# Kernel optimization log

Hardware: AMD Instinct MI355X
Metric: run time of the kernel (lower is better)

Reference implementation:

```python
import jax, jax.numpy as jnp
import numpy as np

B, T, D, HD = 8, 2048, 1024, 64

def setup_inputs() -> dict:
    key = jax.random.key(0)
    k1, k2, k3, k4 = jax.random.split(key, 4)
    x = jax.random.normal(k1, (B, T, D), dtype=jnp.float32)
    Wq = jax.random.normal(k2, (D, HD), dtype=jnp.float32) * (D ** -0.5)
    Wk = jax.random.normal(k3, (D, HD), dtype=jnp.float32) * (D ** -0.5)
    Wv = jax.random.normal(k4, (D, HD), dtype=jnp.float32) * (D ** -0.5)
    return {"x": x, "Wq": Wq, "Wk": Wk, "Wv": Wv}

def reference(x, Wq, Wk, Wv):
    # x: [B,T,D]; projections: [D,HD]
    q = jnp.einsum('btd,dh->bth', x, Wq)
    k = jnp.einsum('btd,dh->bth', x, Wk)
    v = jnp.einsum('btd,dh->bth', x, Wv)
    hd = q.shape[-1]
    scores = jnp.einsum('bth,bsh->bts', q, k) * (hd ** -0.5)  # [B,T,T]
    t = scores.shape[-1]
    causal = jnp.tril(jnp.ones((t, t), dtype=bool))
    scores = jnp.where(causal, scores, -jnp.inf)
    w = jax.nn.softmax(scores, axis=-1)
    # dropout p=0.0 (eval) -> identity
    return jnp.einsum('bts,bsh->bth', w, v)
```

## Files before the change

kernel.cpp:

```cpp
#include <hip/hip_runtime.h>
#include <hip/hip_bf16.h>
#include <stdint.h>

#define NB 8
#define TT 2048
#define DD 1024
#define HDIM 64

typedef __bf16 bf16x8 __attribute__((ext_vector_type(8)));
typedef float f32x4 __attribute__((ext_vector_type(4)));
typedef ushort u16x4 __attribute__((ext_vector_type(4)));

static_assert(sizeof(bf16x8) == 16, "bf16x8 must be 16 bytes");

__device__ inline ushort f2bf_bits(float f) {
    __hip_bfloat16 h = __float2bfloat16(f);
    return *reinterpret_cast<ushort*>(&h);
}
__device__ inline float bfbits2f(ushort u) {
    unsigned v = ((unsigned)u) << 16;
    return __builtin_bit_cast(float, v);
}
__device__ inline bf16x8 ldb8(const ushort* p) {
    return *reinterpret_cast<const bf16x8*>(p);
}

typedef __attribute__((address_space(3))) uint32_t lds_u32;
typedef const __attribute__((address_space(1))) uint32_t glb_u32;
__device__ inline void gl_lds16(const void* g, void* l) {
    __builtin_amdgcn_global_load_lds((glb_u32*)g, (lds_u32*)l, 16, 0, 0);
}

#define WCNT_VM2   0xF72
#define WCNT_VM3   0xF73
#define WCNT_VM5   0xF75
#define WCNT_LGKM0 0xC07F

__device__ inline int probe_f32(const ushort* x) {
    int lane = threadIdx.x & 63;
    int wild = 0;
    #pragma unroll
    for (int j = 0; j < 4; ++j) {
        ushort u = x[(lane * 4 + j) * 32];
        int e = (u >> 7) & 0xFF;
        wild += (e >= 0xC0);
    }
    unsigned long long m = __ballot(wild > 0);
    return __popcll(m) > 8;
}

__global__ __launch_bounds__(256) void k_wt(const ushort* __restrict__ x,
                                            const void* __restrict__ Wq,
                                            const void* __restrict__ Wk,
                                            const void* __restrict__ Wv,
                                            ushort* __restrict__ Wt) {
    int f32m = probe_f32(x);
    int idx = blockIdx.x * 256 + threadIdx.x;
    int mat = idx >> 16;
    int rem = idx & 65535;
    int d = rem >> 6;
    int h = rem & 63;
    const void* W = (mat == 0) ? Wq : (mat == 1) ? Wk : Wv;
    float v;
    if (f32m) v = ((const float*)W)[rem];
    else      v = bfbits2f(((const ushort*)W)[rem]);
    if (mat == 0) v *= 0.18033688011112042f;
    int n    = mat * 64 + h;
    int nt   = n >> 4, ncol = n & 15;
    int kk   = d >> 6, ks = (d >> 5) & 1, qd = (d >> 3) & 3, e = d & 7;
    int f    = nt * 2 + ks;
    Wt[((size_t)(kk * 24 + f)) * 512 + (qd * 16 + ncol) * 8 + e] = f2bf_bits(v);
}

template <int F32M>
__device__ inline void proj_body(const void* __restrict__ xv,
                                 const ushort* __restrict__ Wt,
                                 ushort* __restrict__ Qw,
                                 ushort* __restrict__ Kw,
                                 ushort* __restrict__ Vtw,
                                 ushort* Bf, ushort* Afb) {
    int tid  = threadIdx.x;
    int w    = tid >> 6;
    int lane = tid & 63;
    int quad = lane >> 4;
    int col  = lane & 15;
    int mt   = w >> 2;
    int nh   = w & 3;
    int m0   = blockIdx.x * 64;

    const float*  xf = (const float*)xv;
    const ushort* xb = (const ushort*)xv;

    auto stageB = [&](int buf, int kkk) {
        int kk24 = (kkk >> 6) * 24;
        if (w < 8) {
            #pragma unroll
            for (int j = 0; j < 2; ++j) {
                int f = w * 2 + j;
                gl_lds16(Wt + ((size_t)(kk24 + f)) * 512 + lane * 8,
                         Bf + ((size_t)buf * 24 + f) * 512);
            }
        } else {
            int f = 16 + (w - 8);
            gl_lds16(Wt + ((size_t)(kk24 + f)) * 512 + lane * 8,
                     Bf + ((size_t)buf * 24 + f) * 512);
        }
    };

    int arow = m0 + w * 4 + quad;
    int aa   = (w >> 2) * 2 + (col >> 3);
    int aoff = (((col & 7) >> 1) * 16 + (w & 3) * 4 + quad) * 8
             + (col & 1) * 4;

    f32x4 ar_f;
    u16x4 ar_b;
    auto loadA = [&](int kkk) {
        if (F32M) ar_f = *reinterpret_cast<const f32x4*>(xf + (size_t)arow * DD + kkk + col * 4);
        else      ar_b = *reinterpret_cast<const u16x4*>(xb + (size_t)arow * DD + kkk + col * 4);
    };
    auto writeA = [&](int q) {
        u16x4 v;
        if (F32M) {
            #pragma unroll
            for (int j = 0; j < 4; ++j) v[j] = f2bf_bits(ar_f[j]);
        } else {
            v = ar_b;
        }
        *reinterpret_cast<u16x4*>(Afb + ((size_t)q * 8 + aa) * 512 + aoff) = v;
    };

    f32x4 acc[3];
    #pragma unroll
    for (int i = 0; i < 3; ++i) acc[i] = (f32x4){0.f,0.f,0.f,0.f};

    loadA(0);
    stageB(0, 0);
    stageB(1, 64);
    writeA(0);
    __builtin_amdgcn_s_waitcnt(WCNT_LGKM0);

    for (int t = 0; t < 16; ++t) {
        int p   = t % 3;
        int p2  = (t + 2) % 3;
        int kn1 = (t + 1 < 16) ? (t + 1) * 64 : 960;
        int kn2 = (t + 2 < 16) ? (t + 2) * 64 : 960;
        loadA(kn1);
        stageB(p2, kn2);
        if (w < 8) __builtin_amdgcn_s_waitcnt(WCNT_VM5);
        else       __builtin_amdgcn_s_waitcnt(WCNT_VM3);
        __builtin_amdgcn_s_barrier();

        int q = t & 1;
        #pragma unroll
        for (int ks = 0; ks < 2; ++ks) {
            bf16x8 a = ldb8(Afb + ((size_t)q * 8 + mt * 2 + ks) * 512 + lane * 8);
            #pragma unroll
            for (int j = 0; j < 3; ++j) {
                int nt = nh * 3 + j;
                bf16x8 b = ldb8(Bf + ((size_t)p * 24 + nt * 2 + ks) * 512 + lane * 8);
                acc[j] = __builtin_amdgcn_mfma_f32_16x16x32_bf16(a, b, acc[j], 0, 0, 0);
            }
        }
        writeA(q ^ 1);
        __builtin_amdgcn_s_waitcnt(WCNT_LGKM0);
        __builtin_amdgcn_s_barrier();
    }

    #pragma unroll
    for (int j = 0; j < 3; ++j) {
        int nt  = nh * 3 + j;
        int mat = nt >> 2;
        int h   = (nt & 3) * 16 + col;
        if (mat == 2) {
            #pragma unroll
            for (int r = 0; r < 4; ++r) {
                int row = m0 + mt * 16 + quad * 4 + r;
                int bb = row >> 11;
                int t  = row & (TT - 1);
                Vtw[(size_t)bb * HDIM * TT + (size_t)h * TT + t] = f2bf_bits(acc[j][r]);
            }
        } else {
            ushort* outp = (mat == 0) ? Qw : Kw;
            #pragma unroll
            for (int r = 0; r < 4; ++r) {
                int row = m0 + mt * 16 + quad * 4 + r;
                outp[(size_t)row * HDIM + h] = f2bf_bits(acc[j][r]);
            }
        }
    }
}

__global__ __launch_bounds__(1024) void k_proj(const void* __restrict__ xv,
                                               const ushort* __restrict__ Wt,
                                               ushort* __restrict__ Qw,
                                               ushort* __restrict__ Kw,
                                               ushort* __restrict__ Vtw) {
    __shared__ ushort Bf[3 * 24 * 512];
    __shared__ ushort Afb[2 * 8 * 512];
    if (probe_f32((const ushort*)xv)) proj_body<1>(xv, Wt, Qw, Kw, Vtw, Bf, Afb);
    else                              proj_body<0>(xv, Wt, Qw, Kw, Vtw, Bf, Afb);
}

__global__ __launch_bounds__(256) void k_attn(const ushort* __restrict__ Qw,
                                              const ushort* __restrict__ Kw,
                                              const ushort* __restrict__ Vtw,
                                              ushort* __restrict__ Po,
                                              float* __restrict__ Pl) {
    int w    = threadIdx.x >> 6;
    int lane = threadIdx.x & 63;
    int quad = lane >> 4;
    int col  = lane & 15;
    int bid  = blockIdx.x;
    int b    = bid & 7;
    int idx  = 79 - (bid >> 3);
    int c, g;
    if (idx < 32)      { c = 0; g = idx; }
    else if (idx < 56) { c = 1; g = idx - 24; }
    else if (idx < 72) { c = 2; g = idx - 40; }
    else               { c = 3; g = idx - 48; }
    int qb = 4 * g + w;
    int m0 = qb * 16;
    int Bq = (qb < 32) ? qb : (qb < 64) ? 2*qb - 32 : (qb < 96) ? 3*qb - 96 : 4*qb - 192;
    int pid = b * 320 + Bq + c;

    const ushort* Qb = Qw + (size_t)b * TT * HDIM;
    const ushort* Kb = Kw + (size_t)b * TT * HDIM;
    const ushort* Vb = Vtw + (size_t)b * HDIM * TT;

    __shared__ ushort KVb[2][8][512];
    __shared__ __hip_bfloat16 Pls[4][16][40];

    auto stageKV = [&](int buf, int s) {
        #pragma unroll
        for (int j = 0; j < 2; ++j) {
            int f = w * 2 + j;
            const ushort* gp;
            if (f < 4) {
                int half = f & 1;
                int ro   = (f >> 1) * 16;
                gp = Kb + (size_t)(s + ro + col) * HDIM + half * 32 + quad * 8;
            } else {
                int vg = f - 4;
                gp = Vb + (size_t)(vg * 16 + col) * TT + s + quad * 8;
            }
            gl_lds16(gp, &KVb[buf][f][0]);
        }
    };

    bf16x8 qf0 = ldb8(Qb + (size_t)(m0 + col) * HDIM + quad * 8);
    bf16x8 qf1 = ldb8(Qb + (size_t)(m0 + col) * HDIM + 32 + quad * 8);

    f32x4 o0 = {0.f,0.f,0.f,0.f};
    f32x4 o1 = {0.f,0.f,0.f,0.f};
    f32x4 o2 = {0.f,0.f,0.f,0.f};
    f32x4 o3 = {0.f,0.f,0.f,0.f};
    float rsum[4] = {0.f, 0.f, 0.f, 0.f};

    const int start = c * 512;
    const int end   = min(start + 512, 64 * g + 64);

    stageKV(0, start);
    for (int s0 = start; s0 < end; s0 += 32) {
        int p  = ((s0 - start) >> 5) & 1;
        int sn = (s0 + 32 < end) ? s0 + 32 : s0;
        stageKV(p ^ 1, sn);
        __builtin_amdgcn_s_waitcnt(WCNT_VM2);
        __builtin_amdgcn_s_barrier();

        if (s0 < m0 + 16) {
            bf16x8 ck0l = ldb8(&KVb[p][0][lane * 8]);
            bf16x8 ck0h = ldb8(&KVb[p][1][lane * 8]);
            bf16x8 ck1l = ldb8(&KVb[p][2][lane * 8]);
            bf16x8 ck1h = ldb8(&KVb[p][3][lane * 8]);

            f32x4 S0 = {0.f,0.f,0.f,0.f};
            f32x4 S1 = {0.f,0.f,0.f,0.f};
            S0 = __builtin_amdgcn_mfma_f32_16x16x32_bf16(qf0, ck0l, S0, 0, 0, 0);
            S0 = __builtin_amdgcn_mfma_f32_16x16x32_bf16(qf1, ck0h, S0, 0, 0, 0);
            S1 = __builtin_amdgcn_mfma_f32_16x16x32_bf16(qf0, ck1l, S1, 0, 0, 0);
            S1 = __builtin_amdgcn_mfma_f32_16x16x32_bf16(qf1, ck1h, S1, 0, 0, 0);

            #pragma unroll
            for (int r = 0; r < 4; ++r) {
                int trow = m0 + quad * 4 + r;
                float aa = (s0 + col      > trow) ? -1e30f : S0[r];
                float dd = (s0 + 16 + col > trow) ? -1e30f : S1[r];
                float p0 = exp2f(aa);
                float p1 = exp2f(dd);
                rsum[r] += p0 + p1;
                Pls[w][quad * 4 + r][col]      = __float2bfloat16(p0);
                Pls[w][quad * 4 + r][16 + col] = __float2bfloat16(p1);
            }
            bf16x8 pf = *reinterpret_cast<const bf16x8*>(&Pls[w][col][quad * 8]);

            bf16x8 cv0 = ldb8(&KVb[p][4][lane * 8]);
            bf16x8 cv1 = ldb8(&KVb[p][5][lane * 8]);
            bf16x8 cv2 = ldb8(&KVb[p][6][lane * 8]);
            bf16x8 cv3 = ldb8(&KVb[p][7][lane * 8]);
            o0 = __builtin_amdgcn_mfma_f32_16x16x32_bf16(pf, cv0, o0, 0, 0, 0);
            o1 = __builtin_amdgcn_mfma_f32_16x16x32_bf16(pf, cv1, o1, 0, 0, 0);
            o2 = __builtin_amdgcn_mfma_f32_16x16x32_bf16(pf, cv2, o2, 0, 0, 0);
            o3 = __builtin_amdgcn_mfma_f32_16x16x32_bf16(pf, cv3, o3, 0, 0, 0);
        }
        __builtin_amdgcn_s_waitcnt(WCNT_LGKM0);
        __builtin_amdgcn_s_barrier();
    }

    #pragma unroll
    for (int off = 1; off < 16; off <<= 1) {
        #pragma unroll
        for (int r = 0; r < 4; ++r)
            rsum[r] += __shfl_xor(rsum[r], off, 64);
    }

    ushort* pb = Po + (size_t)pid * 1024;
    #pragma unroll
    for (int r = 0; r < 4; ++r) {
        int row = quad * 4 + r;
        pb[row * 64 + 0*16 + col] = f2bf_bits(o0[r]);
        pb[row * 64 + 1*16 + col] = f2bf_bits(o1[r]);
        pb[row * 64 + 2*16 + col] = f2bf_bits(o2[r]);
        pb[row * 64 + 3*16 + col] = f2bf_bits(o3[r]);
        if (col == 0) Pl[pid * 16 + row] = rsum[r];
    }
}

__global__ __launch_bounds__(256) void k_merge(const ushort* __restrict__ x,
                                               const ushort* __restrict__ Po,
                                               const float* __restrict__ Pl,
                                               void* __restrict__ outv) {
    int f32m = probe_f32(x);
    int wid  = blockIdx.x * 4 + (threadIdx.x >> 6);
    int lane = threadIdx.x & 63;
    int row  = lane >> 2;
    int g    = lane & 3;
    int b    = wid >> 7;
    int qb   = wid & 127;
    int nch  = (qb >> 5) + 1;
    int Bq   = (qb < 32) ? qb : (qb < 64) ? 2*qb - 32 : (qb < 96) ? 3*qb - 96 : 4*qb - 192;
    int pid0 = b * 320 + Bq;

    float L = 0.f;
    #pragma unroll
    for (int c = 0; c < 4; ++c)
        if (c < nch) L += Pl[(pid0 + c) * 16 + row];
    float inv = 1.0f / L;

    float o[16];
    #pragma unroll
    for (int j = 0; j < 16; ++j) o[j] = 0.f;
    #pragma unroll
    for (int c = 0; c < 4; ++c) {
        if (c < nch) {
            const ushort* p = Po + (size_t)(pid0 + c) * 1024 + row * 64 + g * 16;
            bf16x8 v0 = ldb8(p);
            bf16x8 v1 = ldb8(p + 8);
            #pragma unroll
            for (int j = 0; j < 8; ++j) {
                o[j]     += (float)v0[j];
                o[8 + j] += (float)v1[j];
            }
        }
    }

    size_t obase = ((size_t)b * TT + qb * 16 + row) * HDIM + g * 16;
    if (f32m) {
        float* ob = (float*)outv + obase;
        #pragma unroll
        for (int j = 0; j < 16; ++j) ob[j] = o[j] * inv;
    } else {
        ushort* ob = (ushort*)outv + obase;
        #pragma unroll
        for (int j = 0; j < 16; ++j) ob[j] = f2bf_bits(o[j] * inv);
    }
}

extern "C" void kernel_launch(void* const* d_in, const int* in_sizes, int n_in,
                              void* d_out, int out_size, void* d_ws, size_t ws_size,
                              hipStream_t stream) {
    const ushort* x = (const ushort*)d_in[0];
    ushort* Wt  = (ushort*)d_ws;
    ushort* Qw  = Wt + 3 * HDIM * DD;
    ushort* Kw  = Qw + (size_t)NB * TT * HDIM;
    ushort* Vtw = Kw + (size_t)NB * TT * HDIM;
    ushort* Po  = Vtw + (size_t)NB * TT * HDIM;
    float*  Pl  = (float*)(Po + (size_t)2560 * 1024);

    k_wt   <<<768, 256, 0, stream>>>(x, d_in[1], d_in[2], d_in[3], Wt);
    k_proj <<<256, 1024, 0, stream>>>(d_in[0], Wt, Qw, Kw, Vtw);
    k_attn <<<640, 256, 0, stream>>>(Qw, Kw, Vtw, Po, Pl);
    k_merge<<<256, 256, 0, stream>>>(x, Po, Pl, d_out);
}
```

Baseline: 144.6 us.

## Halve projection block to 8 waves with 2 M-tiles per wave, double-buffer B

The QKV projection kernel now runs 512-thread blocks (8 waves) instead of 1024. Each wave computes two 16-row M tiles against three N tiles, so every B fragment read from LDS feeds two MFMAs. B staging drops from triple to double buffering with a uniform 3 loads per wave, and A loading is reorganised so each thread loads two chunks. This cuts LDS traffic and waves per block, but leaves less prefetch depth to hide global latency and raises per-thread register use.

```diff
diff --git a/kernel.cpp b/kernel.cpp
--- a/kernel.cpp
+++ b/kernel.cpp
@@ -32,7 +32,6 @@
 }
 
 #define WCNT_VM2   0xF72
-#define WCNT_VM3   0xF73
 #define WCNT_VM5   0xF75
 #define WCNT_LGKM0 0xC07F
 
@@ -84,7 +83,7 @@
     int lane = tid & 63;
     int quad = lane >> 4;
     int col  = lane & 15;
-    int mt   = w >> 2;
+    int mtw  = w >> 2;
     int nh   = w & 3;
     int m0   = blockIdx.x * 64;
 
@@ -93,110 +92,116 @@
 
     auto stageB = [&](int buf, int kkk) {
         int kk24 = (kkk >> 6) * 24;
-        if (w < 8) {
-            #pragma unroll
-            for (int j = 0; j < 2; ++j) {
-                int f = w * 2 + j;
-                gl_lds16(Wt + ((size_t)(kk24 + f)) * 512 + lane * 8,
-                         Bf + ((size_t)buf * 24 + f) * 512);
-            }
-        } else {
-            int f = 16 + (w - 8);
+        #pragma unroll
+        for (int j = 0; j < 3; ++j) {
+            int f = w * 3 + j;
             gl_lds16(Wt + ((size_t)(kk24 + f)) * 512 + lane * 8,
                      Bf + ((size_t)buf * 24 + f) * 512);
         }
     };
 
-    int arow = m0 + w * 4 + quad;
-    int aa   = (w >> 2) * 2 + (col >> 3);
-    int aoff = (((col & 7) >> 1) * 16 + (w & 3) * 4 + quad) * 8
-             + (col & 1) * 4;
-
-    f32x4 ar_f;
-    u16x4 ar_b;
+    int arow  = m0 + w * 8 + (lane >> 3);
+    int amt_s = w >> 1;
+    int colp  = (w & 1) * 8 + (lane >> 3);
+    f32x4 arf[2];
+    u16x4 arb[2];
     auto loadA = [&](int kkk) {
-        if (F32M) ar_f = *reinterpret_cast<const f32x4*>(xf + (size_t)arow * DD + kkk + col * 4);
-        else      ar_b = *reinterpret_cast<const u16x4*>(xb + (size_t)arow * DD + kkk + col * 4);
+        #pragma unroll
+        for (int i = 0; i < 2; ++i) {
+            int c = (lane & 7) + i * 8;
+            if (F32M) arf[i] = *reinterpret_cast<const f32x4*>(xf + (size_t)arow * DD + kkk + c * 4);
+            else      arb[i] = *reinterpret_cast<const u16x4*>(xb + (size_t)arow * DD + kkk + c * 4);
+        }
     };
     auto writeA = [&](int q) {
-        u16x4 v;
-        if (F32M) {
-            #pragma unroll
-            for (int j = 0; j < 4; ++j) v[j] = f2bf_bits(ar_f[j]);
-        } else {
-            v = ar_b;
-        }
-        *reinterpret_cast<u16x4*>(Afb + ((size_t)q * 8 + aa) * 512 + aoff) = v;
+        #pragma unroll
+        for (int i = 0; i < 2; ++i) {
+            int c  = (lane & 7) + i * 8;
+            int ks = i;
+            int qd = (c & 7) >> 1;
+            int e0 = (c & 1) * 4;
+            u16x4 v;
+            if (F32M) {
+                #pragma unroll
+                for (int j = 0; j < 4; ++j) v[j] = f2bf_bits(arf[i][j]);
+            } else {
+                v = arb[i];
+            }
+            *reinterpret_cast<u16x4*>(Afb + ((size_t)q * 16 + amt_s * 2 + ks) * 512
+                                      + (qd * 16 + colp) * 8 + e0) = v;
+        }
     };
 
-    f32x4 acc[3];
-    #pragma unroll
-    for (int i = 0; i < 3; ++i) acc[i] = (f32x4){0.f,0.f,0.f,0.f};
+    f32x4 acc[2][3];
+    #pragma unroll
+    for (int i = 0; i < 2; ++i)
+        #pragma unroll
+        for (int j = 0; j < 3; ++j) acc[i][j] = (f32x4){0.f, 0.f, 0.f, 0.f};
 
     loadA(0);
     stageB(0, 0);
-    stageB(1, 64);
     writeA(0);
     __builtin_amdgcn_s_waitcnt(WCNT_LGKM0);
 
     for (int t = 0; t < 16; ++t) {
-        int p   = t % 3;
-        int p2  = (t + 2) % 3;
+        int p   = t & 1;
         int kn1 = (t + 1 < 16) ? (t + 1) * 64 : 960;
-        int kn2 = (t + 2 < 16) ? (t + 2) * 64 : 960;
         loadA(kn1);
-        stageB(p2, kn2);
-        if (w < 8) __builtin_amdgcn_s_waitcnt(WCNT_VM5);
-        else       __builtin_amdgcn_s_waitcnt(WCNT_VM3);
+        stageB(p ^ 1, kn1);
+        __builtin_amdgcn_s_waitcnt(WCNT_VM5);
         __builtin_amdgcn_s_barrier();
 
-        int q = t & 1;
         #pragma unroll
         for (int ks = 0; ks < 2; ++ks) {
-            bf16x8 a = ldb8(Afb + ((size_t)q * 8 + mt * 2 + ks) * 512 + lane * 8);
+            bf16x8 a0 = ldb8(Afb + ((size_t)p * 16 + (mtw * 2 + 0) * 2 + ks) * 512 + lane * 8);
+            bf16x8 a1 = ldb8(Afb + ((size_t)p * 16 + (mtw * 2 + 1) * 2 + ks) * 512 + lane * 8);
             #pragma unroll
             for (int j = 0; j < 3; ++j) {
                 int nt = nh * 3 + j;
                 bf16x8 b = ldb8(Bf + ((size_t)p * 24 + nt * 2 + ks) * 512 + lane * 8);
-                acc[j] = __builtin_amdgcn_mfma_f32_16x16x32_bf16(a, b, acc[j], 0, 0, 0);
-            }
-        }
-        writeA(q ^ 1);
+                acc[0][j] = __builtin_amdgcn_mfma_f32_16x16x32_bf16(a0, b, acc[0][j], 0, 0, 0);
+                acc[1][j] = __builtin_amdgcn_mfma_f32_16x16x32_bf16(a1, b, acc[1][j], 0, 0, 0);
+            }
+        }
+        writeA(p ^ 1);
         __builtin_amdgcn_s_waitcnt(WCNT_LGKM0);
         __builtin_amdgcn_s_barrier();
     }
 
     #pragma unroll
-    for (int j = 0; j < 3; ++j) {
-        int nt  = nh * 3 + j;
-        int mat = nt >> 2;
-        int h   = (nt & 3) * 16 + col;
-        if (mat == 2) {
-            #pragma unroll
-            for (int r = 0; r < 4; ++r) {
-                int row = m0 + mt * 16 + quad * 4 + r;
-                int bb = row >> 11;
-                int t  = row & (TT - 1);
-                Vtw[(size_t)bb * HDIM * TT + (size_t)h * TT + t] = f2bf_bits(acc[j][r]);
-            }
-        } else {
-            ushort* outp = (mat == 0) ? Qw : Kw;
-            #pragma unroll
-            for (int r = 0; r < 4; ++r) {
-                int row = m0 + mt * 16 + quad * 4 + r;
-                outp[(size_t)row * HDIM + h] = f2bf_bits(acc[j][r]);
-            }
-        }
-    }
-}
-
-__global__ __launch_bounds__(1024) void k_proj(const void* __restrict__ xv,
-                                               const ushort* __restrict__ Wt,
-                                               ushort* __restrict__ Qw,
-                                               ushort* __restrict__ Kw,
-                                               ushort* __restrict__ Vtw) {
-    __shared__ ushort Bf[3 * 24 * 512];
-    __shared__ ushort Afb[2 * 8 * 512];
+    for (int mloc = 0; mloc < 2; ++mloc) {
+        #pragma unroll
+        for (int j = 0; j < 3; ++j) {
+            int nt  = nh * 3 + j;
+            int mat = nt >> 2;
+            int h   = (nt & 3) * 16 + col;
+            if (mat == 2) {
+                #pragma unroll
+                for (int r = 0; r < 4; ++r) {
+                    int row = m0 + mtw * 32 + mloc * 16 + quad * 4 + r;
+                    int bb = row >> 11;
+                    int t  = row & (TT - 1);
+                    Vtw[(size_t)bb * HDIM * TT + (size_t)h * TT + t] = f2bf_bits(acc[mloc][j][r]);
+                }
+            } else {
+                ushort* outp = (mat == 0) ? Qw : Kw;
+                #pragma unroll
+                for (int r = 0; r < 4; ++r) {
+                    int row = m0 + mtw * 32 + mloc * 16 + quad * 4 + r;
+                    outp[(size_t)row * HDIM + h] = f2bf_bits(acc[mloc][j][r]);
+                }
+            }
+        }
+    }
+}
+
+__global__ __launch_bounds__(512, 4) void k_proj(const void* __restrict__ xv,
+                                                 const ushort* __restrict__ Wt,
+                                                 ushort* __restrict__ Qw,
+                                                 ushort* __restrict__ Kw,
+                                                 ushort* __restrict__ Vtw) {
+    __shared__ ushort Bf[2 * 24 * 512];
+    __shared__ ushort Afb[2 * 16 * 512];
     if (probe_f32((const ushort*)xv)) proj_body<1>(xv, Wt, Qw, Kw, Vtw, Bf, Afb);
     else                              proj_body<0>(xv, Wt, Qw, Kw, Vtw, Bf, Afb);
 }
@@ -387,7 +392,7 @@
     float*  Pl  = (float*)(Po + (size_t)2560 * 1024);
 
     k_wt   <<<768, 256, 0, stream>>>(x, d_in[1], d_in[2], d_in[3], Wt);
-    k_proj <<<256, 1024, 0, stream>>>(d_in[0], Wt, Qw, Kw, Vtw);
+    k_proj <<<256, 512, 0, stream>>>(d_in[0], Wt, Qw, Kw, Vtw);
     k_attn <<<640, 256, 0, stream>>>(Qw, Kw, Vtw, Po, Pl);
     k_merge<<<256, 256, 0, stream>>>(x, Po, Pl, d_out);
 }
```

Measured after the change: 144.7 us. About the same (+0.1%).
